# Performance work log

Measured on AMD Instinct MI355X. Metric: run time of the kernel, lower is better.

Reference implementation:

```python
import jax, jax.numpy as jnp
import numpy as np
from jax import lax

STRIDES = [4, 8, 16, 32, 64]
SIZES = [32.0, 64.0, 128.0, 256.0, 512.0]
RATIOS = [0.5, 1.0, 2.0]
IMG_H = IMG_W = 1024.0
NMS_T = 0.7
PRE = 1000      # PRE_NMS_TOPK_TEST
POST = 1000     # POST_NMS_TOPK_TEST
MIN_SIZE = 0.0
N = 2
FEAT = [(256, 256), (128, 128), (64, 64), (32, 32), (16, 16)]
SCALE_CLAMP = float(np.log(1000.0 / 16.0))


def make_anchors(H, W, stride, size):
    # detectron2 DefaultAnchorGenerator: area=size^2, w=sqrt(area/r), h=w*r; grid offsets = stride*arange
    r = np.array(RATIOS)
    ws = np.sqrt(size * size / r)
    hs = ws * r
    base = np.stack([-ws / 2, -hs / 2, ws / 2, hs / 2], axis=1)  # [A,4]
    sx = np.arange(W) * stride
    sy = np.arange(H) * stride
    yy, xx = np.meshgrid(sy, sx, indexing='ij')
    shifts = np.stack([xx, yy, xx, yy], axis=-1).reshape(-1, 1, 4)  # [H*W,1,4]
    return jnp.asarray((shifts + base[None]).reshape(-1, 4), jnp.float32)  # [H*W*A,4]


def conv2d(x, w, b, pad):
    y = lax.conv_general_dilated(x, w, (1, 1), [(pad, pad), (pad, pad)],
                                 dimension_numbers=('NCHW', 'OIHW', 'NCHW'))
    return y + b[None, :, None, None]


def apply_deltas(deltas, anchors):
    # Box2BoxTransform.apply_deltas with weights (1,1,1,1)
    w = anchors[..., 2] - anchors[..., 0]
    h = anchors[..., 3] - anchors[..., 1]
    cx = anchors[..., 0] + 0.5 * w
    cy = anchors[..., 1] + 0.5 * h
    dx, dy, dw, dh = deltas[..., 0], deltas[..., 1], deltas[..., 2], deltas[..., 3]
    dw = jnp.minimum(dw, SCALE_CLAMP)
    dh = jnp.minimum(dh, SCALE_CLAMP)
    pcx = dx * w + cx
    pcy = dy * h + cy
    pw = jnp.exp(dw) * w
    ph = jnp.exp(dh) * h
    return jnp.stack([pcx - 0.5 * pw, pcy - 0.5 * ph, pcx + 0.5 * pw, pcy + 0.5 * ph], axis=-1)


def pairwise_iou(b):
    area = (b[:, 2] - b[:, 0]) * (b[:, 3] - b[:, 1])
    lt = jnp.maximum(b[:, None, :2], b[None, :, :2])
    rb = jnp.minimum(b[:, None, 2:], b[None, :, 2:])
    wh = jnp.clip(rb - lt, 0.0)
    inter = wh[..., 0] * wh[..., 1]
    return inter / jnp.maximum(area[:, None] + area[None, :] - inter, 1e-9)


def nms_keep(boxes, valid):
    # boxes already sorted by score desc; sequential greedy NMS keep mask
    K = boxes.shape[0]
    M = pairwise_iou(boxes)
    idx = jnp.arange(K)

    def body(i, keep):
        sup = (M[i] > NMS_T) & (idx > i) & keep[i]
        return keep & (~sup)

    return lax.fori_loop(0, K, body, valid)


def rpn_forward(feats, conv_w, conv_b, obj_w, obj_b, delta_w, delta_b):
    all_boxes, all_scores = [], []
    lim = jnp.array([IMG_W, IMG_H, IMG_W, IMG_H], jnp.float32)
    for x, (H, W), stride, size in zip(feats, FEAT, STRIDES, SIZES):
        t = jax.nn.relu(conv2d(x, conv_w, conv_b, 1))
        logits = conv2d(t, obj_w, obj_b, 0)      # [N,A,H,W]
        deltas = conv2d(t, delta_w, delta_b, 0)  # [N,4A,H,W]
        A = logits.shape[1]
        logits = logits.transpose(0, 2, 3, 1).reshape(N, -1)                       # [N,H*W*A]
        deltas = deltas.reshape(N, A, 4, H, W).transpose(0, 3, 4, 1, 2).reshape(N, -1, 4)
        anchors = make_anchors(H, W, stride, size)
        props = apply_deltas(deltas, anchors[None])                                # [N,H*W*A,4]
        k = min(PRE, props.shape[1])
        scores, idx = lax.top_k(logits, k)                                         # [N,k]
        boxes = jnp.take_along_axis(props, idx[..., None], axis=1)                 # [N,k,4]
        boxes = jnp.clip(boxes, 0.0, lim)                                          # clip to image
        valid = ((boxes[..., 2] - boxes[..., 0]) > MIN_SIZE) & ((boxes[..., 3] - boxes[..., 1]) > MIN_SIZE)
        keep = lax.stop_gradient(jax.vmap(nms_keep)(boxes, valid))                 # NMS is no_grad in torch
        all_boxes.append(boxes)
        all_scores.append(jnp.where(keep, scores, -1e9))
    boxes = jnp.concatenate(all_boxes, axis=1)
    scores = jnp.concatenate(all_scores, axis=1)
    fs, fi = lax.top_k(scores, POST)                                               # final sort-by-score
    fb = jnp.take_along_axis(boxes, fi[..., None], axis=1)
    return fb, fs


def setup_inputs() -> dict:
    key = jax.random.key(0)
    ks = jax.random.split(key, 8)
    d = {}
    for i, (name, (H, W)) in enumerate(zip(['p2', 'p3', 'p4', 'p5', 'p6'], FEAT)):
        d[name] = jax.random.normal(ks[i], (N, 256, H, W), jnp.float32)
    d['conv_w'] = jax.random.normal(ks[5], (256, 256, 3, 3), jnp.float32) * 0.01
    d['conv_b'] = jnp.zeros((256,), jnp.float32)
    d['obj_w'] = jax.random.normal(ks[6], (3, 256, 1, 1), jnp.float32) * 0.01
    d['obj_b'] = jnp.zeros((3,), jnp.float32)
    d['delta_w'] = jax.random.normal(ks[7], (12, 256, 1, 1), jnp.float32) * 0.01
    d['delta_b'] = jnp.zeros((12,), jnp.float32)
    return d


def reference(p2, p3, p4, p5, p6, conv_w, conv_b, obj_w, obj_b, delta_w, delta_b):
    return rpn_forward([p2, p3, p4, p5, p6], conv_w, conv_b, obj_w, obj_b, delta_w, delta_b)
```

## Files before the change

### kernel.cpp

```cpp
#include <hip/hip_runtime.h>
#include <stdint.h>

#define DEVI __device__ __forceinline__

#define S_TOT 261888
#define NIMG  2
#define SCLD  4.135166556742356

__constant__ int    c_S[5]    = {196608, 49152, 12288, 3072, 768};
__constant__ int    c_loff[5] = {0, 196608, 245760, 258048, 261120};
__constant__ int    c_K[5]    = {1000, 1000, 1000, 1000, 768};
__constant__ int    c_Wl[5]   = {256, 128, 64, 32, 16};
__constant__ int    c_str[5]  = {4, 8, 16, 32, 64};
__constant__ double c_sz[5]   = {32.0, 64.0, 128.0, 256.0, 512.0};
__constant__ double c_rat[3]  = {0.5, 1.0, 2.0};
__constant__ int    c_boff[6] = {0, 256, 320, 336, 340, 341};
__constant__ int    c_Hl[5]   = {256, 128, 64, 32, 16};

DEVI unsigned key_of(float f) {
  unsigned u = __float_as_uint(f);
  return (u & 0x80000000u) ? ~u : (u | 0x80000000u);
}
DEVI float key_dec(unsigned k) {
  unsigned u = (k & 0x80000000u) ? (k & 0x7fffffffu) : ~k;
  return __uint_as_float(u);
}

__global__ void transpose_w(const float* __restrict__ w, float* __restrict__ wT2) {
  int k  = blockIdx.x;
  int co = threadIdx.x;
  int ci = k / 9, j = k - ci * 9;
  wT2[((size_t)(ci * 16 + (co >> 4))) * 144 + j * 16 + (co & 15)] = w[co * 2304 + k];
}

__global__ __launch_bounds__(512, 4) void conv_fused(
    const float* __restrict__ x0, const float* __restrict__ x1,
    const float* __restrict__ x2, const float* __restrict__ x3,
    const float* __restrict__ x4,
    const float* __restrict__ wT2,
    const float* __restrict__ cb, const float* __restrict__ ow,
    const float* __restrict__ ob, const float* __restrict__ dwt,
    const float* __restrict__ db, float* __restrict__ logits,
    float* __restrict__ deltas)
{
  __shared__ float lds[7680];
  const int tid = threadIdx.x;
  const int n = blockIdx.y;
  const int b = blockIdx.x;
  int l = 0;
#pragma unroll
  for (int q = 1; q < 5; ++q) if (b >= c_boff[q]) l = q;
  const int t = b - c_boff[l];
  const int H = c_Hl[l], W = H;
  const int tilesx = 16 >> l;
  const int tx = t & (tilesx - 1), ty = t >> (4 - l);
  const int px0 = tx << 4, py0 = ty << 4;
  const int loff = c_loff[l];
  const float* xin = (l == 0) ? x0 : (l == 1) ? x1 : (l == 2) ? x2 : (l == 3) ? x3 : x4;
  xin += (size_t)n * 256 * H * W;

  const int lane = tid & 63, wv = tid >> 6;
  const int px = lane & 15, p = lane >> 4;

  for (int pass = 0; pass < 2; ++pass) {
    const int g = (pass << 3) + __builtin_amdgcn_readfirstlane(wv);
    const int co0 = g << 4;

    float acc[4][16];
#pragma unroll
    for (int k = 0; k < 4; ++k)
#pragma unroll
      for (int i = 0; i < 16; ++i) acc[k][i] = 0.f;

    for (int ch = 0; ch < 16; ++ch) {
      const int ci0 = ch << 4;
      __syncthreads();
      for (int tt = tid; tt < 16 * 324; tt += 512) {
        int ci = tt / 324, rem = tt - ci * 324;
        int ry = rem / 18, rx = rem - ry * 18;
        int gy = py0 + ry - 1, gx = px0 + rx - 1;
        float v = 0.f;
        if (gy >= 0 && gy < H && gx >= 0 && gx < W)
          v = xin[((size_t)(ci0 + ci) * H + gy) * W + gx];
        lds[tt] = v;
      }
      __syncthreads();
#pragma unroll 1
      for (int cc = 0; cc < 16; ++cc) {
        const int pb = cc * 324 + p * 18 + px;
        const float* wr = wT2 + ((size_t)((ci0 + cc) * 16 + g)) * 144;
#pragma unroll
        for (int ky = 0; ky < 3; ++ky) {
          float pvk[4][3];
#pragma unroll
          for (int k = 0; k < 4; ++k)
#pragma unroll
            for (int kx = 0; kx < 3; ++kx)
              pvk[k][kx] = lds[pb + ((k << 2) + ky) * 18 + kx];
#pragma unroll
          for (int kx = 0; kx < 3; ++kx) {
#pragma unroll
            for (int i = 0; i < 16; ++i) {
              const float wgt = wr[(ky * 3 + kx) * 16 + i];
#pragma unroll
              for (int k = 0; k < 4; ++k)
                acc[k][i] = fmaf(wgt, pvk[k][kx], acc[k][i]);
            }
          }
        }
      }
    }

#pragma unroll 1
    for (int k = 0; k < 4; ++k) {
      float part[15];
#pragma unroll
      for (int f = 0; f < 15; ++f) part[f] = 0.f;
#pragma unroll
      for (int i = 0; i < 16; ++i) {
        float tv = fmaxf(acc[k][i] + cb[co0 + i], 0.f);
#pragma unroll
        for (int f = 0; f < 3; ++f)  part[f]     = fmaf(tv, ow[f * 256 + co0 + i],  part[f]);
#pragma unroll
        for (int f = 0; f < 12; ++f) part[3 + f] = fmaf(tv, dwt[f * 256 + co0 + i], part[3 + f]);
      }
      __syncthreads();
#pragma unroll
      for (int f = 0; f < 15; ++f) lds[wv * 960 + f * 64 + lane] = part[f];
      __syncthreads();
      for (int tt = tid; tt < 960; tt += 512) {
        int f = tt >> 6, pp = tt & 63;
        int gx = px0 + (pp & 15), gy = py0 + (pp >> 4) + (k << 2);
        int cell = gy * W + gx;
        size_t adr;
        float bias;
        if (f < 3) {
          adr = (size_t)n * S_TOT + loff + cell * 3 + f;
          bias = ob[f];
        } else {
          int chn = f - 3, a = chn >> 2, c = chn & 3;
          adr = (((size_t)n * S_TOT + loff + cell * 3 + a) << 2) + c;
          bias = db[chn];
        }
        float* dst = (f < 3) ? logits : deltas;
        float s = (pass == 0) ? 0.f : dst[adr];
#pragma unroll
        for (int w2 = 0; w2 < 8; ++w2) s += lds[w2 * 960 + tt];
        dst[adr] = (pass == 0) ? s : (s + bias);
      }
    }
  }
}

__global__ __launch_bounds__(1024) void topk_kernel(
    const float* __restrict__ logits, const float* __restrict__ deltas,
    float* __restrict__ selscore, float* __restrict__ selbox,
    unsigned* __restrict__ selvalid)
{
  const int tid = threadIdx.x;
  const int nl = blockIdx.x, n = nl / 5, l = nl % 5;
  const int Sl = c_S[l], loff = c_loff[l], Kl = c_K[l], Wl = c_Wl[l], strl = c_str[l];
  const float* sc = logits + (size_t)n * S_TOT + loff;

  __shared__ unsigned hist[256];
  __shared__ unsigned sh_prefix, sh_need, s_base, s_cb;
  __shared__ unsigned waveTot[16], waveOff[16];
  __shared__ unsigned long long sortbuf[1024];

  unsigned prefix = 0, need = (unsigned)Kl;
  for (int p = 0; p < 4; ++p) {
    for (int i = tid; i < 256; i += 1024) hist[i] = 0;
    __syncthreads();
    const int shift = 24 - p * 8;
    for (int i = tid; i < Sl; i += 1024) {
      unsigned k = key_of(sc[i]);
      if (p == 0 || (k >> (shift + 8)) == prefix)
        atomicAdd(&hist[(k >> shift) & 255u], 1u);
    }
    __syncthreads();
    if (tid == 0) {
      unsigned cum = 0;
      for (int b = 255; b >= 0; --b) {
        unsigned c = hist[b];
        if (cum + c >= need) { sh_prefix = (prefix << 8) | (unsigned)b; sh_need = need - cum; break; }
        cum += c;
      }
    }
    __syncthreads();
    prefix = sh_prefix; need = sh_need;
    __syncthreads();
  }
  const unsigned Tkey = prefix;

  if (tid == 0) s_base = 0;
  __syncthreads();
  for (int pass = 0; pass < 2; ++pass) {
    for (int st = 0; st < Sl; st += 1024) {
      const int i = st + tid;
      bool flag = false; unsigned k = 0;
      if (i < Sl) {
        k = key_of(sc[i]);
        flag = (pass == 0) ? (k > Tkey) : (k == Tkey);
      }
      unsigned long long m = __ballot(flag);
      const int lane = tid & 63, w = tid >> 6;
      unsigned mypre = (unsigned)__popcll(m & ((1ull << lane) - 1ull));
      if (lane == 0) waveTot[w] = (unsigned)__popcll(m);
      __syncthreads();
      if (tid == 0) {
        unsigned ss = 0;
        for (int q = 0; q < 16; ++q) { waveOff[q] = ss; ss += waveTot[q]; }
        s_cb = s_base; s_base += ss;
      }
      __syncthreads();
      if (flag) {
        unsigned pos = s_cb + waveOff[w] + mypre;
        if (pos < (unsigned)Kl)
          sortbuf[pos] = (((unsigned long long)k) << 32) |
                         (unsigned long long)(0xFFFFFFFFu - (unsigned)i);
      }
      __syncthreads();
    }
  }
  if (tid >= Kl) sortbuf[tid] = (unsigned long long)(0xFFFFFFFFu - (unsigned)tid);
  __syncthreads();

  for (int k2 = 2; k2 <= 1024; k2 <<= 1) {
    for (int j = k2 >> 1; j > 0; j >>= 1) {
      const int i = tid, ixj = i ^ j;
      if (ixj > i) {
        unsigned long long a = sortbuf[i], b = sortbuf[ixj];
        const bool desc = (i & k2) == 0;
        if (desc ? (a < b) : (a > b)) { sortbuf[i] = b; sortbuf[ixj] = a; }
      }
      __syncthreads();
    }
  }

  const int r = tid;
  const int o = nl * 1024 + r;
  if (r < Kl) {
    unsigned long long v = sortbuf[r];
    unsigned k = (unsigned)(v >> 32);
    unsigned ai = 0xFFFFFFFFu - (unsigned)(v & 0xFFFFFFFFull);
    float score = key_dec(k);
    int cell = (int)(ai / 3u), a = (int)(ai % 3u);
    int xg = cell % Wl, yg = cell / Wl;
    double rr = c_rat[a], sz = c_sz[l];
    double wsd = sqrt(sz * sz / rr);
    double hw = 0.5 * wsd, hh = 0.5 * wsd * rr;
    double xs = (double)(xg * strl), ys = (double)(yg * strl);
    float a0 = (float)(xs - hw), a1 = (float)(ys - hh);
    float a2 = (float)(xs + hw), a3 = (float)(ys + hh);
    const float* dp = deltas + (((size_t)n * S_TOT + loff + ai) << 2);
    float dx = dp[0], dy = dp[1], dw_ = dp[2], dh_ = dp[3];
    float aw = a2 - a0, ah = a3 - a1;
    float cx = a0 + 0.5f * aw, cy = a1 + 0.5f * ah;
    dw_ = fminf(dw_, (float)SCLD); dh_ = fminf(dh_, (float)SCLD);
    float pcx = dx * aw + cx, pcy = dy * ah + cy;
    float pw = expf(dw_) * aw, ph = expf(dh_) * ah;
    float b0 = fminf(fmaxf(pcx - 0.5f * pw, 0.f), 1024.f);
    float b1 = fminf(fmaxf(pcy - 0.5f * ph, 0.f), 1024.f);
    float b2 = fminf(fmaxf(pcx + 0.5f * pw, 0.f), 1024.f);
    float b3 = fminf(fmaxf(pcy + 0.5f * ph, 0.f), 1024.f);
    unsigned valid = ((b2 - b0) > 0.f && (b3 - b1) > 0.f) ? 1u : 0u;
    selscore[o] = score;
    selbox[o * 4 + 0] = b0; selbox[o * 4 + 1] = b1;
    selbox[o * 4 + 2] = b2; selbox[o * 4 + 3] = b3;
    selvalid[o] = valid;
  } else {
    selscore[o] = -1e9f;
    selbox[o * 4 + 0] = 0.f; selbox[o * 4 + 1] = 0.f;
    selbox[o * 4 + 2] = 0.f; selbox[o * 4 + 3] = 0.f;
    selvalid[o] = 0u;
  }
}

__global__ __launch_bounds__(256) void nms_sup(
    const float* __restrict__ selbox, unsigned long long* __restrict__ sup)
{
  int gid = blockIdx.x * 256 + threadIdx.x;
  int w = gid & 15, i = (gid >> 4) & 1023, nl = gid >> 14;
  if (nl >= 10) return;
  int l = nl % 5, Kl = c_K[l];
  unsigned long long bits = 0;
  if (i < Kl) {
    const float* bi = selbox + (size_t)(nl * 1024 + i) * 4;
    float x0 = bi[0], y0 = bi[1], x1 = bi[2], y1 = bi[3];
    float ar = (x1 - x0) * (y1 - y0);
    int jlo = w * 64; if (jlo < i + 1) jlo = i + 1;
    int jhi = w * 64 + 64; if (jhi > Kl) jhi = Kl;
    for (int j = jlo; j < jhi; ++j) {
      const float* bj = selbox + (size_t)(nl * 1024 + j) * 4;
      float u0 = fmaxf(x0, bj[0]), v0 = fmaxf(y0, bj[1]);
      float u1 = fminf(x1, bj[2]), v1 = fminf(y1, bj[3]);
      float iw = fmaxf(u1 - u0, 0.f), ih = fmaxf(v1 - v0, 0.f);
      float inter = iw * ih;
      float aj = (bj[2] - bj[0]) * (bj[3] - bj[1]);
      float iou = inter / fmaxf(ar + aj - inter, 1e-9f);
      if (iou > 0.7f) bits |= 1ull << (j - w * 64);
    }
  }
  sup[(size_t)(nl * 1024 + i) * 16 + w] = bits;
}

__global__ __launch_bounds__(64) void nms_reduce(
    const unsigned* __restrict__ selvalid, const unsigned long long* __restrict__ sup,
    const float* __restrict__ selscore, float* __restrict__ scnms)
{
  const int nl = blockIdx.x, tid = threadIdx.x;
  const int l = nl % 5, Kl = c_K[l];
  unsigned long long keep = 0;
  if (tid < 16) {
    for (int t = 0; t < 64; ++t) {
      int r = tid * 64 + t;
      if (r < Kl && selvalid[nl * 1024 + r]) keep |= 1ull << t;
    }
  }
  const unsigned long long* srow = sup + (size_t)nl * 1024 * 16;
  unsigned long long rowA = (tid < 16) ? srow[(size_t)0 * 16 + tid] : 0;
  unsigned long long rowB = (tid < 16 && Kl > 1) ? srow[(size_t)1 * 16 + tid] : 0;
  for (int i = 0; i < Kl; i += 2) {
    unsigned long long kw = __shfl(keep, i >> 6);
    unsigned long long cur = rowA;
    rowA = (tid < 16 && i + 2 < Kl) ? srow[(size_t)(i + 2) * 16 + tid] : 0;
    if (((kw >> (i & 63)) & 1ull) && tid < 16) keep &= ~cur;
    kw = __shfl(keep, (i + 1) >> 6);
    cur = rowB;
    rowB = (tid < 16 && i + 3 < Kl) ? srow[(size_t)(i + 3) * 16 + tid] : 0;
    if (((kw >> ((i + 1) & 63)) & 1ull) && tid < 16) keep &= ~cur;
  }
  for (int r = tid; r < 1024; r += 64) {
    unsigned long long wv = __shfl(keep, r >> 6);
    bool kp = (r < Kl) && ((wv >> (r & 63)) & 1ull);
    scnms[nl * 1024 + r] = kp ? selscore[nl * 1024 + r] : -1e9f;
  }
}

DEVI float cand_score(const float* scnms, int n, int g) {
  int l = g / 1000;
  int r = g - l * 1000;
  return scnms[((n * 5 + l) << 10) + r];
}

__global__ __launch_bounds__(1024) void final_topk(
    const float* __restrict__ scnms, const float* __restrict__ selbox,
    float* __restrict__ out)
{
  const int tid = threadIdx.x;
  const int n = blockIdx.x;
  const int S = 4768;

  __shared__ unsigned hist[256];
  __shared__ unsigned sh_prefix, sh_need, s_base, s_cb;
  __shared__ unsigned waveTot[16], waveOff[16];
  __shared__ unsigned long long sortbuf[1024];

  unsigned prefix = 0, need = 1000;
  for (int p = 0; p < 4; ++p) {
    for (int i = tid; i < 256; i += 1024) hist[i] = 0;
    __syncthreads();
    const int shift = 24 - p * 8;
    for (int i = tid; i < S; i += 1024) {
      unsigned k = key_of(cand_score(scnms, n, i));
      if (p == 0 || (k >> (shift + 8)) == prefix)
        atomicAdd(&hist[(k >> shift) & 255u], 1u);
    }
    __syncthreads();
    if (tid == 0) {
      unsigned cum = 0;
      for (int b = 255; b >= 0; --b) {
        unsigned c = hist[b];
        if (cum + c >= need) { sh_prefix = (prefix << 8) | (unsigned)b; sh_need = need - cum; break; }
        cum += c;
      }
    }
    __syncthreads();
    prefix = sh_prefix; need = sh_need;
    __syncthreads();
  }
  const unsigned Tkey = prefix;

  if (tid == 0) s_base = 0;
  __syncthreads();
  for (int pass = 0; pass < 2; ++pass) {
    for (int st = 0; st < S; st += 1024) {
      const int i = st + tid;
      bool flag = false; unsigned k = 0;
      if (i < S) {
        k = key_of(cand_score(scnms, n, i));
        flag = (pass == 0) ? (k > Tkey) : (k == Tkey);
      }
      unsigned long long m = __ballot(flag);
      const int lane = tid & 63, w = tid >> 6;
      unsigned mypre = (unsigned)__popcll(m & ((1ull << lane) - 1ull));
      if (lane == 0) waveTot[w] = (unsigned)__popcll(m);
      __syncthreads();
      if (tid == 0) {
        unsigned ss = 0;
        for (int q = 0; q < 16; ++q) { waveOff[q] = ss; ss += waveTot[q]; }
        s_cb = s_base; s_base += ss;
      }
      __syncthreads();
      if (flag) {
        unsigned pos = s_cb + waveOff[w] + mypre;
        if (pos < 1000u)
          sortbuf[pos] = (((unsigned long long)k) << 32) |
                         (unsigned long long)(0xFFFFFFFFu - (unsigned)i);
      }
      __syncthreads();
    }
  }
  if (tid >= 1000) sortbuf[tid] = (unsigned long long)(0xFFFFFFFFu - (unsigned)tid);
  __syncthreads();

  for (int k2 = 2; k2 <= 1024; k2 <<= 1) {
    for (int j = k2 >> 1; j > 0; j >>= 1) {
      const int i = tid, ixj = i ^ j;
      if (ixj > i) {
        unsigned long long a = sortbuf[i], b = sortbuf[ixj];
        const bool desc = (i & k2) == 0;
        if (desc ? (a < b) : (a > b)) { sortbuf[i] = b; sortbuf[ixj] = a; }
      }
      __syncthreads();
    }
  }

  if (tid < 1000) {
    unsigned long long v = sortbuf[tid];
    unsigned k = (unsigned)(v >> 32);
    int g = (int)(0xFFFFFFFFu - (unsigned)(v & 0xFFFFFFFFull));
    int l = g / 1000, r = g - l * 1000;
    const float* b = selbox + ((size_t)((n * 5 + l) * 1024 + r)) * 4;
    size_t ob_ = ((size_t)n * 1000 + tid) * 4;
    out[ob_ + 0] = b[0]; out[ob_ + 1] = b[1];
    out[ob_ + 2] = b[2]; out[ob_ + 3] = b[3];
    out[8000 + n * 1000 + tid] = key_dec(k);
  }
}

extern "C" void kernel_launch(void* const* d_in, const int* in_sizes, int n_in,
                              void* d_out, int out_size, void* d_ws, size_t ws_size,
                              hipStream_t stream)
{
  const float* feats[5];
  for (int i = 0; i < 5; ++i) feats[i] = (const float*)d_in[i];
  const float* conv_w  = (const float*)d_in[5];
  const float* conv_b  = (const float*)d_in[6];
  const float* obj_w   = (const float*)d_in[7];
  const float* obj_b   = (const float*)d_in[8];
  const float* delta_w = (const float*)d_in[9];
  const float* delta_b = (const float*)d_in[10];

  char* wsp = (char*)d_ws;
  float* wT2      = (float*)wsp;  wsp += (size_t)2304 * 256 * 4;
  float* logits   = (float*)wsp;  wsp += (size_t)NIMG * S_TOT * 4;
  float* deltas   = (float*)wsp;  wsp += (size_t)NIMG * S_TOT * 16;
  float* selscore = (float*)wsp;  wsp += (size_t)10 * 1024 * 4;
  float* selbox   = (float*)wsp;  wsp += (size_t)10 * 1024 * 16;
  unsigned* selvalid = (unsigned*)wsp; wsp += (size_t)10 * 1024 * 4;
  float* scnms    = (float*)wsp;  wsp += (size_t)10 * 1024 * 4;
  unsigned long long* sup = (unsigned long long*)wsp;
  wsp += (size_t)10 * 1024 * 16 * 8;

  transpose_w<<<dim3(2304), dim3(256), 0, stream>>>(conv_w, wT2);

  conv_fused<<<dim3(341, NIMG), dim3(512), 0, stream>>>(
      feats[0], feats[1], feats[2], feats[3], feats[4],
      wT2, conv_b, obj_w, obj_b, delta_w, delta_b, logits, deltas);

  topk_kernel<<<dim3(10), dim3(1024), 0, stream>>>(logits, deltas,
                                                   selscore, selbox, selvalid);
  nms_sup<<<dim3(640), dim3(256), 0, stream>>>(selbox, sup);
  nms_reduce<<<dim3(10), dim3(64), 0, stream>>>(selvalid, sup, selscore, scnms);
  final_topk<<<dim3(NIMG), dim3(1024), 0, stream>>>(scnms, selbox, (float*)d_out);
}
```

Measured before the change: 3.736 ms.

## Stage conv weights in LDS per 8-channel chunk with float4 reads

```diff
diff --git a/kernel.cpp b/kernel.cpp
--- a/kernel.cpp
+++ b/kernel.cpp
@@ -26,24 +26,28 @@
   return __uint_as_float(u);
 }
 
-__global__ void transpose_w(const float* __restrict__ w, float* __restrict__ wT2) {
+__global__ void transpose_w(const float* __restrict__ w, float* __restrict__ wT3) {
   int k  = blockIdx.x;
   int co = threadIdx.x;
   int ci = k / 9, j = k - ci * 9;
-  wT2[((size_t)(ci * 16 + (co >> 4))) * 144 + j * 16 + (co & 15)] = w[co * 2304 + k];
+  int chunk = ci >> 3, cc = ci & 7;
+  int pass = co >> 7, g = (co >> 4) & 7, i = co & 15;
+  wT3[((size_t)(pass * 32 + chunk)) * 9216 + cc * 1152 + g * 144 + j * 16 + i] =
+      w[co * 2304 + k];
 }
 
 __global__ __launch_bounds__(512, 4) void conv_fused(
     const float* __restrict__ x0, const float* __restrict__ x1,
     const float* __restrict__ x2, const float* __restrict__ x3,
     const float* __restrict__ x4,
-    const float* __restrict__ wT2,
+    const float* __restrict__ wT3,
     const float* __restrict__ cb, const float* __restrict__ ow,
     const float* __restrict__ ob, const float* __restrict__ dwt,
     const float* __restrict__ db, float* __restrict__ logits,
     float* __restrict__ deltas)
 {
-  __shared__ float lds[7680];
+  __shared__ float lds[11808];
+  float* const wlds = lds + 2592;
   const int tid = threadIdx.x;
   const int n = blockIdx.y;
   const int b = blockIdx.x;
@@ -63,8 +67,8 @@
   const int px = lane & 15, p = lane >> 4;
 
   for (int pass = 0; pass < 2; ++pass) {
-    const int g = (pass << 3) + __builtin_amdgcn_readfirstlane(wv);
-    const int co0 = g << 4;
+    const int g = wv;
+    const int co0 = (pass << 7) + (g << 4);
 
     float acc[4][16];
 #pragma unroll
@@ -72,10 +76,10 @@
 #pragma unroll
       for (int i = 0; i < 16; ++i) acc[k][i] = 0.f;
 
-    for (int ch = 0; ch < 16; ++ch) {
-      const int ci0 = ch << 4;
-      __syncthreads();
-      for (int tt = tid; tt < 16 * 324; tt += 512) {
+    for (int ch = 0; ch < 32; ++ch) {
+      const int ci0 = ch << 3;
+      __syncthreads();
+      for (int tt = tid; tt < 2592; tt += 512) {
         int ci = tt / 324, rem = tt - ci * 324;
         int ry = rem / 18, rx = rem - ry * 18;
         int gy = py0 + ry - 1, gx = px0 + rx - 1;
@@ -84,11 +88,16 @@
           v = xin[((size_t)(ci0 + ci) * H + gy) * W + gx];
         lds[tt] = v;
       }
+      {
+        const float4* wg = (const float4*)(wT3 + ((size_t)(pass * 32 + ch)) * 9216);
+        float4* wl = (float4*)wlds;
+        for (int tt = tid; tt < 2304; tt += 512) wl[tt] = wg[tt];
+      }
       __syncthreads();
 #pragma unroll 1
-      for (int cc = 0; cc < 16; ++cc) {
+      for (int cc = 0; cc < 8; ++cc) {
         const int pb = cc * 324 + p * 18 + px;
-        const float* wr = wT2 + ((size_t)((ci0 + cc) * 16 + g)) * 144;
+        const float* wr = wlds + cc * 1152 + g * 144;
 #pragma unroll
         for (int ky = 0; ky < 3; ++ky) {
           float pvk[4][3];
@@ -99,19 +108,35 @@
               pvk[k][kx] = lds[pb + ((k << 2) + ky) * 18 + kx];
 #pragma unroll
           for (int kx = 0; kx < 3; ++kx) {
-#pragma unroll
-            for (int i = 0; i < 16; ++i) {
-              const float wgt = wr[(ky * 3 + kx) * 16 + i];
-#pragma unroll
-              for (int k = 0; k < 4; ++k)
-                acc[k][i] = fmaf(wgt, pvk[k][kx], acc[k][i]);
+            const float4 w0 = *(const float4*)(wr + (ky * 3 + kx) * 16 + 0);
+            const float4 w1 = *(const float4*)(wr + (ky * 3 + kx) * 16 + 4);
+            const float4 w2 = *(const float4*)(wr + (ky * 3 + kx) * 16 + 8);
+            const float4 w3 = *(const float4*)(wr + (ky * 3 + kx) * 16 + 12);
+#pragma unroll
+            for (int k = 0; k < 4; ++k) {
+              acc[k][0]  = fmaf(w0.x, pvk[k][kx], acc[k][0]);
+              acc[k][1]  = fmaf(w0.y, pvk[k][kx], acc[k][1]);
+              acc[k][2]  = fmaf(w0.z, pvk[k][kx], acc[k][2]);
+              acc[k][3]  = fmaf(w0.w, pvk[k][kx], acc[k][3]);
+              acc[k][4]  = fmaf(w1.x, pvk[k][kx], acc[k][4]);
+              acc[k][5]  = fmaf(w1.y, pvk[k][kx], acc[k][5]);
+              acc[k][6]  = fmaf(w1.z, pvk[k][kx], acc[k][6]);
+              acc[k][7]  = fmaf(w1.w, pvk[k][kx], acc[k][7]);
+              acc[k][8]  = fmaf(w2.x, pvk[k][kx], acc[k][8]);
+              acc[k][9]  = fmaf(w2.y, pvk[k][kx], acc[k][9]);
+              acc[k][10] = fmaf(w2.z, pvk[k][kx], acc[k][10]);
+              acc[k][11] = fmaf(w2.w, pvk[k][kx], acc[k][11]);
+              acc[k][12] = fmaf(w3.x, pvk[k][kx], acc[k][12]);
+              acc[k][13] = fmaf(w3.y, pvk[k][kx], acc[k][13]);
+              acc[k][14] = fmaf(w3.z, pvk[k][kx], acc[k][14]);
+              acc[k][15] = fmaf(w3.w, pvk[k][kx], acc[k][15]);
             }
           }
         }
       }
     }
 
-#pragma unroll 1
+#pragma unroll
     for (int k = 0; k < 4; ++k) {
       float part[15];
 #pragma unroll
@@ -453,7 +478,7 @@
   const float* delta_b = (const float*)d_in[10];
 
   char* wsp = (char*)d_ws;
-  float* wT2      = (float*)wsp;  wsp += (size_t)2304 * 256 * 4;
+  float* wT3      = (float*)wsp;  wsp += (size_t)2304 * 256 * 4;
   float* logits   = (float*)wsp;  wsp += (size_t)NIMG * S_TOT * 4;
   float* deltas   = (float*)wsp;  wsp += (size_t)NIMG * S_TOT * 16;
   float* selscore = (float*)wsp;  wsp += (size_t)10 * 1024 * 4;
@@ -463,11 +488,11 @@
   unsigned long long* sup = (unsigned long long*)wsp;
   wsp += (size_t)10 * 1024 * 16 * 8;
 
-  transpose_w<<<dim3(2304), dim3(256), 0, stream>>>(conv_w, wT2);
+  transpose_w<<<dim3(2304), dim3(256), 0, stream>>>(conv_w, wT3);
 
   conv_fused<<<dim3(341, NIMG), dim3(512), 0, stream>>>(
       feats[0], feats[1], feats[2], feats[3], feats[4],
-      wT2, conv_b, obj_w, obj_b, delta_w, delta_b, logits, deltas);
+      wT3, conv_b, obj_w, obj_b, delta_w, delta_b, logits, deltas);
 
   topk_kernel<<<dim3(10), dim3(1024), 0, stream>>>(logits, deltas,
                                                    selscore, selbox, selvalid);
```

New measurement: 4.893 ms. 1.31x slower.

## Retile 3x3 conv to 16x32 pixel tiles with LDS-staged weights and register blocking

Applied to the files above, without the earlier changes.

```diff
diff --git a/kernel.cpp b/kernel.cpp
--- a/kernel.cpp
+++ b/kernel.cpp
@@ -14,7 +14,7 @@
 __constant__ int    c_str[5]  = {4, 8, 16, 32, 64};
 __constant__ double c_sz[5]   = {32.0, 64.0, 128.0, 256.0, 512.0};
 __constant__ double c_rat[3]  = {0.5, 1.0, 2.0};
-__constant__ int    c_boff[6] = {0, 256, 320, 336, 340, 341};
+__constant__ int    c_boff[6] = {0, 128, 160, 168, 170, 171};
 __constant__ int    c_Hl[5]   = {256, 128, 64, 32, 16};
 
 DEVI unsigned key_of(float f) {
@@ -26,24 +26,28 @@
   return __uint_as_float(u);
 }
 
-__global__ void transpose_w(const float* __restrict__ w, float* __restrict__ wT2) {
+__global__ void transpose_w(const float* __restrict__ w, float* __restrict__ wT7) {
   int k  = blockIdx.x;
   int co = threadIdx.x;
   int ci = k / 9, j = k - ci * 9;
-  wT2[((size_t)(ci * 16 + (co >> 4))) * 144 + j * 16 + (co & 15)] = w[co * 2304 + k];
+  int chunk = ci >> 2, cc = ci & 3;
+  int pass = co >> 6, wvv = (co >> 3) & 7, i = co & 7;
+  wT7[((size_t)((pass * 64 + chunk) * 4 + cc)) * 576 + wvv * 72 + j * 8 + i] =
+      w[co * 2304 + k];
 }
 
 __global__ __launch_bounds__(512, 4) void conv_fused(
     const float* __restrict__ x0, const float* __restrict__ x1,
     const float* __restrict__ x2, const float* __restrict__ x3,
     const float* __restrict__ x4,
-    const float* __restrict__ wT2,
+    const float* __restrict__ wT7,
     const float* __restrict__ cb, const float* __restrict__ ow,
     const float* __restrict__ ob, const float* __restrict__ dwt,
     const float* __restrict__ db, float* __restrict__ logits,
     float* __restrict__ deltas)
 {
   __shared__ float lds[7680];
+  float* const wlds = lds + 2592;
   const int tid = threadIdx.x;
   const int n = blockIdx.y;
   const int b = blockIdx.x;
@@ -54,7 +58,7 @@
   const int H = c_Hl[l], W = H;
   const int tilesx = 16 >> l;
   const int tx = t & (tilesx - 1), ty = t >> (4 - l);
-  const int px0 = tx << 4, py0 = ty << 4;
+  const int px0 = tx << 4, py0 = ty << 5;
   const int loff = c_loff[l];
   const float* xin = (l == 0) ? x0 : (l == 1) ? x1 : (l == 2) ? x2 : (l == 3) ? x3 : x4;
   xin += (size_t)n * 256 * H * W;
@@ -62,63 +66,77 @@
   const int lane = tid & 63, wv = tid >> 6;
   const int px = lane & 15, p = lane >> 4;
 
-  for (int pass = 0; pass < 2; ++pass) {
-    const int g = (pass << 3) + __builtin_amdgcn_readfirstlane(wv);
-    const int co0 = g << 4;
-
-    float acc[4][16];
-#pragma unroll
-    for (int k = 0; k < 4; ++k)
-#pragma unroll
-      for (int i = 0; i < 16; ++i) acc[k][i] = 0.f;
-
-    for (int ch = 0; ch < 16; ++ch) {
-      const int ci0 = ch << 4;
-      __syncthreads();
-      for (int tt = tid; tt < 16 * 324; tt += 512) {
-        int ci = tt / 324, rem = tt - ci * 324;
+#pragma unroll 1
+  for (int pass = 0; pass < 4; ++pass) {
+    float acc[64];
+#pragma unroll
+    for (int i = 0; i < 64; ++i) acc[i] = 0.f;
+
+    for (int ch = 0; ch < 64; ++ch) {
+      const int ci0 = ch << 2;
+      __syncthreads();
+      for (int tt = tid; tt < 2448; tt += 512) {
+        int ci = tt / 612, rem = tt - ci * 612;
         int ry = rem / 18, rx = rem - ry * 18;
         int gy = py0 + ry - 1, gx = px0 + rx - 1;
         float v = 0.f;
         if (gy >= 0 && gy < H && gx >= 0 && gx < W)
           v = xin[((size_t)(ci0 + ci) * H + gy) * W + gx];
-        lds[tt] = v;
+        lds[ci * 648 + rx * 36 + ry] = v;
+      }
+      {
+        const float4* wg = (const float4*)(wT7 + (size_t)(pass * 64 + ch) * 2304);
+        float4* wl = (float4*)wlds;
+        for (int tt = tid; tt < 576; tt += 512) wl[tt] = wg[tt];
       }
       __syncthreads();
 #pragma unroll 1
-      for (int cc = 0; cc < 16; ++cc) {
-        const int pb = cc * 324 + p * 18 + px;
-        const float* wr = wT2 + ((size_t)((ci0 + cc) * 16 + g)) * 144;
+      for (int cc = 0; cc < 4; ++cc) {
+        const float* wr = wlds + cc * 576 + wv * 72;
+        const int pb = cc * 648 + px * 36 + (p << 3);
+        float c0[10], c1[10], c2[10];
+        *(float4*)&c0[0] = *(const float4*)&lds[pb +  0];
+        *(float4*)&c0[4] = *(const float4*)&lds[pb +  4];
+        *(float2*)&c0[8] = *(const float2*)&lds[pb +  8];
+        *(float4*)&c1[0] = *(const float4*)&lds[pb + 36];
+        *(float4*)&c1[4] = *(const float4*)&lds[pb + 40];
+        *(float2*)&c1[8] = *(const float2*)&lds[pb + 44];
+        *(float4*)&c2[0] = *(const float4*)&lds[pb + 72];
+        *(float4*)&c2[4] = *(const float4*)&lds[pb + 76];
+        *(float2*)&c2[8] = *(const float2*)&lds[pb + 80];
 #pragma unroll
         for (int ky = 0; ky < 3; ++ky) {
-          float pvk[4][3];
-#pragma unroll
-          for (int k = 0; k < 4; ++k)
-#pragma unroll
-            for (int kx = 0; kx < 3; ++kx)
-              pvk[k][kx] = lds[pb + ((k << 2) + ky) * 18 + kx];
 #pragma unroll
           for (int kx = 0; kx < 3; ++kx) {
-#pragma unroll
-            for (int i = 0; i < 16; ++i) {
-              const float wgt = wr[(ky * 3 + kx) * 16 + i];
-#pragma unroll
-              for (int k = 0; k < 4; ++k)
-                acc[k][i] = fmaf(wgt, pvk[k][kx], acc[k][i]);
+            const float* wt = wr + (ky * 3 + kx) * 8;
+            const float4 wa = *(const float4*)(wt + 0);
+            const float4 wb = *(const float4*)(wt + 4);
+#pragma unroll
+            for (int r = 0; r < 8; ++r) {
+              const float v = (kx == 0) ? c0[r + ky] : (kx == 1) ? c1[r + ky] : c2[r + ky];
+              acc[r * 8 + 0] = fmaf(wa.x, v, acc[r * 8 + 0]);
+              acc[r * 8 + 1] = fmaf(wa.y, v, acc[r * 8 + 1]);
+              acc[r * 8 + 2] = fmaf(wa.z, v, acc[r * 8 + 2]);
+              acc[r * 8 + 3] = fmaf(wa.w, v, acc[r * 8 + 3]);
+              acc[r * 8 + 4] = fmaf(wb.x, v, acc[r * 8 + 4]);
+              acc[r * 8 + 5] = fmaf(wb.y, v, acc[r * 8 + 5]);
+              acc[r * 8 + 6] = fmaf(wb.z, v, acc[r * 8 + 6]);
+              acc[r * 8 + 7] = fmaf(wb.w, v, acc[r * 8 + 7]);
             }
           }
         }
       }
     }
 
-#pragma unroll 1
-    for (int k = 0; k < 4; ++k) {
+    const int co0 = __builtin_amdgcn_readfirstlane((pass << 6) + (wv << 3));
+#pragma unroll
+    for (int h = 0; h < 8; ++h) {
       float part[15];
 #pragma unroll
       for (int f = 0; f < 15; ++f) part[f] = 0.f;
 #pragma unroll
-      for (int i = 0; i < 16; ++i) {
-        float tv = fmaxf(acc[k][i] + cb[co0 + i], 0.f);
+      for (int i = 0; i < 8; ++i) {
+        float tv = fmaxf(acc[h * 8 + i] + cb[co0 + i], 0.f);
 #pragma unroll
         for (int f = 0; f < 3; ++f)  part[f]     = fmaf(tv, ow[f * 256 + co0 + i],  part[f]);
 #pragma unroll
@@ -130,23 +148,22 @@
       __syncthreads();
       for (int tt = tid; tt < 960; tt += 512) {
         int f = tt >> 6, pp = tt & 63;
-        int gx = px0 + (pp & 15), gy = py0 + (pp >> 4) + (k << 2);
-        int cell = gy * W + gx;
-        size_t adr;
-        float bias;
-        if (f < 3) {
-          adr = (size_t)n * S_TOT + loff + cell * 3 + f;
-          bias = ob[f];
-        } else {
-          int chn = f - 3, a = chn >> 2, c = chn & 3;
-          adr = (((size_t)n * S_TOT + loff + cell * 3 + a) << 2) + c;
-          bias = db[chn];
+        int gx = px0 + (pp & 15), gy = py0 + ((pp >> 4) << 3) + h;
+        if (gy < H) {
+          int cell = gy * W + gx;
+          size_t adr; float bias; float* dst;
+          if (f < 3) {
+            dst = logits; adr = (size_t)n * S_TOT + loff + cell * 3 + f; bias = ob[f];
+          } else {
+            int chn = f - 3, a = chn >> 2, c = chn & 3;
+            dst = deltas; adr = (((size_t)n * S_TOT + loff + cell * 3 + a) << 2) + c;
+            bias = db[chn];
+          }
+          float s = (pass == 0) ? 0.f : dst[adr];
+#pragma unroll
+          for (int w2 = 0; w2 < 8; ++w2) s += lds[w2 * 960 + tt];
+          dst[adr] = (pass == 3) ? (s + bias) : s;
         }
-        float* dst = (f < 3) ? logits : deltas;
-        float s = (pass == 0) ? 0.f : dst[adr];
-#pragma unroll
-        for (int w2 = 0; w2 < 8; ++w2) s += lds[w2 * 960 + tt];
-        dst[adr] = (pass == 0) ? s : (s + bias);
       }
     }
   }
@@ -453,7 +470,7 @@
   const float* delta_b = (const float*)d_in[10];
 
   char* wsp = (char*)d_ws;
-  float* wT2      = (float*)wsp;  wsp += (size_t)2304 * 256 * 4;
+  float* wT7      = (float*)wsp;  wsp += (size_t)2304 * 256 * 4;
   float* logits   = (float*)wsp;  wsp += (size_t)NIMG * S_TOT * 4;
   float* deltas   = (float*)wsp;  wsp += (size_t)NIMG * S_TOT * 16;
   float* selscore = (float*)wsp;  wsp += (size_t)10 * 1024 * 4;
@@ -463,11 +480,11 @@
   unsigned long long* sup = (unsigned long long*)wsp;
   wsp += (size_t)10 * 1024 * 16 * 8;
 
-  transpose_w<<<dim3(2304), dim3(256), 0, stream>>>(conv_w, wT2);
-
-  conv_fused<<<dim3(341, NIMG), dim3(512), 0, stream>>>(
+  transpose_w<<<dim3(2304), dim3(256), 0, stream>>>(conv_w, wT7);
+
+  conv_fused<<<dim3(171, NIMG), dim3(512), 0, stream>>>(
       feats[0], feats[1], feats[2], feats[3], feats[4],
-      wT2, conv_b, obj_w, obj_b, delta_w, delta_b, logits, deltas);
+      wT7, conv_b, obj_w, obj_b, delta_w, delta_b, logits, deltas);
 
   topk_kernel<<<dim3(10), dim3(1024), 0, stream>>>(logits, deltas,
                                                    selscore, selbox, selvalid);
```

Result: slower. 8.997 ms (+140.8%).
